# Kernel optimization log

Hardware: AMD Instinct MI355X
Metric: run time of the kernel (lower is better)

Reference implementation:

```python
import jax, jax.numpy as jnp
import numpy as np

NUM_HEADS = 12

def setup_inputs() -> dict:
    key = jax.random.key(0)
    k1, k2, k3 = jax.random.split(key, 3)
    B, N, C = 8, 1024, 768
    x = jax.random.normal(k1, (B, N, C), dtype=jnp.float32)
    Wqkv = jax.random.normal(k2, (C, 3 * C), dtype=jnp.float32) * (C ** -0.5)
    bqkv = jnp.zeros((3 * C,), dtype=jnp.float32)
    Wproj = jax.random.normal(k3, (C, C), dtype=jnp.float32) * (C ** -0.5)
    bproj = jnp.zeros((C,), dtype=jnp.float32)
    return {"x": x, "Wqkv": Wqkv, "bqkv": bqkv, "Wproj": Wproj, "bproj": bproj}

def reference(x, Wqkv, bqkv, Wproj, bproj):
    B, N, C = x.shape
    H = NUM_HEADS
    D = C // H
    scale = D ** -0.5
    qkv = x @ Wqkv + bqkv                       # [B,N,3C]
    qkv = qkv.reshape(B, N, 3, H, D)
    q, k, v = qkv[:, :, 0], qkv[:, :, 1], qkv[:, :, 2]  # [B,N,H,D]
    attn = jnp.einsum('bnhd,bmhd->bhnm', q, k) * scale  # [B,H,N,N]
    attn = jax.nn.softmax(attn, axis=-1)
    # dropout is identity in eval mode
    out = jnp.einsum('bhnm,bmhd->bnhd', attn, v).reshape(B, N, C)
    out = out @ Wproj + bproj
    return out
```

## Files before the change

kernel.cpp:

```cpp
#include <hip/hip_runtime.h>
#include <hip/hip_bf16.h>
#include <cstdint>
#include <cstddef>

typedef __bf16 bf16;
typedef __bf16 bf16x8 __attribute__((ext_vector_type(8)));
typedef __bf16 bf16x4 __attribute__((ext_vector_type(4)));
typedef __bf16 bf16x2 __attribute__((ext_vector_type(2)));
typedef float f32x4 __attribute__((ext_vector_type(4)));
typedef float f32x16 __attribute__((ext_vector_type(16)));
typedef unsigned int u32;
typedef u32 u32x4 __attribute__((ext_vector_type(4)));

#define LDS_CAST(p) (__attribute__((address_space(3))) void*)(p)
#define GLB_CAST(p) (const __attribute__((address_space(1))) void*)(p)
#define MFMA16(a, b, c) __builtin_amdgcn_mfma_f32_16x16x32_bf16(a, b, c, 0, 0, 0)
#define MFMA32(a, b, c) __builtin_amdgcn_mfma_f32_32x32x16_bf16(a, b, c, 0, 0, 0)

#if __has_builtin(__builtin_amdgcn_exp2f)
#define EXPF(x) __builtin_amdgcn_exp2f(x)
#define QK_SCALE 0.18033688011112042f
#else
#define EXPF(x) __expf(x)
#define QK_SCALE 0.125f
#endif

static constexpr int BATCH = 8;
static constexpr int NSEQ  = 1024;
static constexpr int CDIM  = 768;
static constexpr int NH    = 12;
static constexpr int HD    = 64;
static constexpr int MTOT  = BATCH * NSEQ;
static constexpr int NC3   = 3 * CDIM;

static constexpr float M_FIX = 12.0f;

__device__ inline u32 pkbf(float a, float b) {
    bf16x2 t = { (bf16)a, (bf16)b };
    return __builtin_bit_cast(u32, t);
}

__global__ void cast_kernel(const float* __restrict__ src, bf16* __restrict__ dst, int n4) {
    int i = blockIdx.x * blockDim.x + threadIdx.x;
    if (i < n4) {
        float4 v = ((const float4*)src)[i];
        bf16x4 o = { (bf16)v.x, (bf16)v.y, (bf16)v.z, (bf16)v.w };
        ((bf16x4*)dst)[i] = o;
    }
}

__global__ void tcast_kernel(const float* __restrict__ src, bf16* __restrict__ dst,
                             int K, int N) {
    __shared__ float tile[32][33];
    const int n0 = blockIdx.x * 32, k0 = blockIdx.y * 32;
    const int tx = threadIdx.x & 31, ty = threadIdx.x >> 5;
#pragma unroll
    for (int p = 0; p < 4; p++)
        tile[ty + p * 8][tx] = src[(size_t)(k0 + ty + p * 8) * N + n0 + tx];
    __syncthreads();
#pragma unroll
    for (int p = 0; p < 4; p++)
        dst[(size_t)(n0 + ty + p * 8) * K + k0 + tx] = (bf16)tile[tx][ty + p * 8];
}

template <int MODE>
__global__ __launch_bounds__(512, 4) void gemm_kernel(
    const bf16* __restrict__ A, const bf16* __restrict__ Bt,
    const float* __restrict__ bias, float* __restrict__ outf,
    bf16* __restrict__ q, bf16* __restrict__ kk, bf16* __restrict__ v,
    int Ndim, int K)
{
    __shared__ alignas(16) bf16 sAB[3][12288];
    const int tid  = threadIdx.x;
    const int lane = tid & 63;
    const int quad = lane >> 4;
    const int l16  = lane & 15;
    const int wid  = tid >> 6;
    const int wmI  = wid >> 1;
    const int wnI  = wid & 1;

    const int wg = blockIdx.x;
    const int x  = (wg & 7) * (gridDim.x >> 3) + (wg >> 3);
    const int nTn = Ndim >> 7;
    const int tn = x % nTn, tm = x / nTn;
    const int tmB = tm << 8, tnB = tn << 7;

    int aoff[4], boff[4];
    {
        const int xr = ((quad ^ (l16 & 3)) << 3);
#pragma unroll
        for (int i = 0; i < 4; i++) aoff[i] = (wmI * 64 + i * 16 + l16) * 32 + xr;
#pragma unroll
        for (int j = 0; j < 4; j++) boff[j] = 8192 + (wnI * 64 + j * 16 + l16) * 32 + xr;
    }

    const int r0 = tid >> 2;
    const int c0 = (tid & 3) ^ (r0 & 3);
    const bf16* gA0 = A  + (size_t)(tmB + r0) * K + c0 * 8;
    const bf16* gA1 = gA0 + (size_t)128 * K;
    const bf16* gB0 = Bt + (size_t)(tnB + r0) * K + c0 * 8;
    const int ldsb = (tid & 448) * 8;

    auto STAGE = [&](int t, int bsel) {
        const int k0 = t << 5;
        bf16* d = &sAB[bsel][0];
        __builtin_amdgcn_global_load_lds(GLB_CAST(gA0 + k0), LDS_CAST(d + ldsb),        16, 0, 0);
        __builtin_amdgcn_global_load_lds(GLB_CAST(gA1 + k0), LDS_CAST(d + 4096 + ldsb), 16, 0, 0);
        __builtin_amdgcn_global_load_lds(GLB_CAST(gB0 + k0), LDS_CAST(d + 8192 + ldsb), 16, 0, 0);
    };

    const f32x4 fzero = {0.f, 0.f, 0.f, 0.f};
    f32x4 acc[4][4];
#pragma unroll
    for (int i = 0; i < 4; i++)
#pragma unroll
        for (int j = 0; j < 4; j++) acc[i][j] = fzero;

    const int NT = K >> 5;
    STAGE(0, 0);
    STAGE(1, 1);
    asm volatile("s_waitcnt vmcnt(3)" ::: "memory");
    __builtin_amdgcn_sched_barrier(0);
    __builtin_amdgcn_s_barrier();

    int bsel = 0;
    for (int t = 0; t < NT; ++t) {
        int b2 = bsel + 2; if (b2 >= 3) b2 -= 3;
        if (t + 2 < NT) STAGE(t + 2, b2);

        const bf16* buf = &sAB[bsel][0];
        bf16x8 af[4], bfr[4];
#pragma unroll
        for (int i = 0; i < 4; i++) af[i]  = *(const bf16x8*)(buf + aoff[i]);
#pragma unroll
        for (int j = 0; j < 4; j++) bfr[j] = *(const bf16x8*)(buf + boff[j]);

        __builtin_amdgcn_s_setprio(1);
#pragma unroll
        for (int i = 0; i < 4; i++)
#pragma unroll
            for (int j = 0; j < 4; j++) acc[i][j] = MFMA16(af[i], bfr[j], acc[i][j]);
        __builtin_amdgcn_s_setprio(0);

        if (t < NT - 1) {
            if (t + 2 < NT) asm volatile("s_waitcnt vmcnt(3)" ::: "memory");
            else            asm volatile("s_waitcnt vmcnt(0)" ::: "memory");
            __builtin_amdgcn_sched_barrier(0);
            __builtin_amdgcn_s_barrier();
            __builtin_amdgcn_sched_barrier(0);
        }
        bsel += 1; if (bsel >= 3) bsel -= 3;
    }

    if (MODE == 0) {
#pragma unroll
        for (int i = 0; i < 4; i++) {
            int row = tmB + wmI * 64 + i * 16 + quad * 4;
#pragma unroll
            for (int j = 0; j < 4; j++) {
                int col = tnB + wnI * 64 + j * 16 + l16;
                float bv = bias[col];
                float* op = outf + (size_t)row * Ndim + col;
#pragma unroll
                for (int r = 0; r < 4; r++) op[(size_t)r * Ndim] = acc[i][j][r] + bv;
            }
        }
    } else {
#pragma unroll
        for (int i = 0; i < 4; i++) {
            int row = tmB + wmI * 64 + i * 16 + quad * 4;
            int b  = row >> 10;
            int ns = row & 1023;
#pragma unroll
            for (int j = 0; j < 4; j++) {
                int col = tnB + wnI * 64 + j * 16 + l16;
                int t3  = col / 768;
                int rem = col - t3 * 768;
                int h = rem >> 6;
                int d = rem & 63;
                float bv = bias[col];
                if (t3 == 0) {
                    bf16* qp = q + ((size_t)(b * NH + h) * NSEQ + ns) * HD + d;
#pragma unroll
                    for (int r = 0; r < 4; r++)
                        qp[(size_t)r * HD] = (bf16)((acc[i][j][r] + bv) * (float)QK_SCALE);
                } else if (t3 == 1) {
                    bf16* kp = kk + ((size_t)(b * NH + h) * NSEQ + ns) * HD + d;
#pragma unroll
                    for (int r = 0; r < 4; r++) kp[(size_t)r * HD] = (bf16)(acc[i][j][r] + bv);
                } else {
                    bf16x4 pv = { (bf16)(acc[i][j][0] + bv), (bf16)(acc[i][j][1] + bv),
                                  (bf16)(acc[i][j][2] + bv), (bf16)(acc[i][j][3] + bv) };
                    *(bf16x4*)(v + ((size_t)(b * NH + h) * HD + d) * NSEQ + ns) = pv;
                }
            }
        }
    }
}

__global__ __launch_bounds__(256) void attn_kernel(
    const bf16* __restrict__ q, const bf16* __restrict__ k,
    const bf16* __restrict__ v, bf16* __restrict__ o)
{
    __shared__ alignas(16) bf16 sKV[2][8192];
    const int tid  = threadIdx.x;
    const int lane = tid & 63;
    const int w    = tid >> 6;
    const int h    = lane >> 5;
    const int l32  = lane & 31;

    const int wg  = blockIdx.x;
    const int xcd = wg & 7;
    const int idx = wg >> 3;
    const int bh  = xcd * 12 + (idx % 12);
    const int qt  = idx / 12;
    const int b = bh / NH, hh = bh - b * NH;

    const bf16* qb = q + ((size_t)bh * NSEQ + qt * 128) * HD;
    const bf16* kb = k + (size_t)bh * NSEQ * HD;
    const bf16* vb = v + (size_t)bh * HD * NSEQ;

#pragma unroll
    for (int i = 0; i < 4; i++) {
        int slot = w * 256 + i * 64 + lane;
        int r = slot >> 3, cs = slot & 7;
        __builtin_amdgcn_global_load_lds(GLB_CAST(qb + r * HD + ((cs ^ (r & 7)) * 8)),
                                         LDS_CAST(&sKV[1][(w * 256 + i * 64) * 8]), 16, 0, 0);
    }
    auto stageKV = [&](int kt, int buf) {
#pragma unroll
        for (int i = 0; i < 2; i++) {
            int slot = w * 128 + i * 64 + lane;
            int r = slot >> 3, cs = slot & 7;
            int cc = (cs ^ (r & 7)) * 8;
            __builtin_amdgcn_global_load_lds(GLB_CAST(kb + (size_t)(kt * 64 + r) * HD + cc),
                                             LDS_CAST(&sKV[buf][(w * 128 + i * 64) * 8]), 16, 0, 0);
            __builtin_amdgcn_global_load_lds(GLB_CAST(vb + (size_t)r * NSEQ + kt * 64 + cc),
                                             LDS_CAST(&sKV[buf][4096 + (w * 128 + i * 64) * 8]), 16, 0, 0);
        }
    };
    stageKV(0, 0);
    __syncthreads();

    bf16x8 qf[4];
    {
        int row = w * 32 + l32, rx = row & 7;
#pragma unroll
        for (int cd = 0; cd < 4; cd++)
            qf[cd] = *(const bf16x8*)(&sKV[1][(row * 8 + ((2 * cd + h) ^ rx)) * 8]);
    }

    bf16x8 onesA;
#pragma unroll
    for (int i = 0; i < 8; i++) onesA[i] = (bf16)1.0f;

    f32x16 accO[2], accL;
#pragma unroll
    for (int dt = 0; dt < 2; dt++)
#pragma unroll
        for (int i = 0; i < 16; i++) accO[dt][i] = 0.f;
#pragma unroll
    for (int i = 0; i < 16; i++) accL[i] = 0.f;

    for (int kt = 0; kt < 16; kt++) {
        const int cur = kt & 1;
        __syncthreads();
        if (kt < 15) stageKV(kt + 1, 1 - cur);
        const bf16* sKc = &sKV[cur][0];
        const bf16* sVc = &sKV[cur][4096];

        f32x16 accS[2];
#pragma unroll
        for (int kvt = 0; kvt < 2; kvt++)
#pragma unroll
            for (int i = 0; i < 16; i++) accS[kvt][i] = 0.f;
        __builtin_amdgcn_s_setprio(1);
#pragma unroll
        for (int kvt = 0; kvt < 2; kvt++) {
            int row = kvt * 32 + l32, rx = row & 7;
#pragma unroll
            for (int cd = 0; cd < 4; cd++) {
                bf16x8 kf = *(const bf16x8*)(sKc + (row * 8 + ((2 * cd + h) ^ rx)) * 8);
                accS[kvt] = MFMA32(kf, qf[cd], accS[kvt]);
            }
        }
        __builtin_amdgcn_s_setprio(0);

        u32 pr[2][4][2];
#pragma unroll
        for (int kvt = 0; kvt < 2; kvt++)
#pragma unroll
            for (int g = 0; g < 4; g++) {
                pr[kvt][g][0] = pkbf(EXPF(accS[kvt][4 * g + 0] - M_FIX),
                                     EXPF(accS[kvt][4 * g + 1] - M_FIX));
                pr[kvt][g][1] = pkbf(EXPF(accS[kvt][4 * g + 2] - M_FIX),
                                     EXPF(accS[kvt][4 * g + 3] - M_FIX));
            }

        bf16x8 pf[4];
#pragma unroll
        for (int c = 0; c < 4; c++) {
            int kvt = c >> 1, c1 = c & 1;
            u32 u00 = pr[kvt][2 * c1][0],     u01 = pr[kvt][2 * c1][1];
            u32 u10 = pr[kvt][2 * c1 + 1][0], u11 = pr[kvt][2 * c1 + 1][1];
            u32 y0 = h ? u10 : u00, y1 = h ? u11 : u01;
            u32 z0 = h ? u00 : u10, z1 = h ? u01 : u11;
            u32 w0 = (u32)__shfl_xor((int)z0, 32);
            u32 w1 = (u32)__shfl_xor((int)z1, 32);
            u32x4 fv = { h ? w0 : y0, h ? w1 : y1, h ? y0 : w0, h ? y1 : w1 };
            pf[c] = __builtin_bit_cast(bf16x8, fv);
        }

        __builtin_amdgcn_s_setprio(1);
#pragma unroll
        for (int dt = 0; dt < 2; dt++) {
            int row = dt * 32 + l32, rx = row & 7;
#pragma unroll
            for (int c = 0; c < 4; c++) {
                bf16x8 vf = *(const bf16x8*)(sVc + (row * 8 + ((2 * c + h) ^ rx)) * 8);
                accO[dt] = MFMA32(vf, pf[c], accO[dt]);
            }
        }
#pragma unroll
        for (int c = 0; c < 4; c++) accL = MFMA32(onesA, pf[c], accL);
        __builtin_amdgcn_s_setprio(0);
    }

    float inv = 1.f / accL[0];
    bf16* ob = o + ((size_t)b * NSEQ + qt * 128 + w * 32 + l32) * CDIM + hh * HD;
#pragma unroll
    for (int dt = 0; dt < 2; dt++)
#pragma unroll
        for (int g = 0; g < 4; g++) {
            bf16x4 t = { (bf16)(accO[dt][4 * g + 0] * inv), (bf16)(accO[dt][4 * g + 1] * inv),
                         (bf16)(accO[dt][4 * g + 2] * inv), (bf16)(accO[dt][4 * g + 3] * inv) };
            *(bf16x4*)(ob + dt * 32 + 8 * g + 4 * h) = t;
        }
}

extern "C" void kernel_launch(void* const* d_in, const int* in_sizes, int n_in,
                              void* d_out, int out_size, void* d_ws, size_t ws_size,
                              hipStream_t stream)
{
    const float* x     = (const float*)d_in[0];
    const float* Wqkv  = (const float*)d_in[1];
    const float* bqkv  = (const float*)d_in[2];
    const float* Wproj = (const float*)d_in[3];
    const float* bproj = (const float*)d_in[4];
    float* out = (float*)d_out;

    char* ws = (char*)d_ws;
    const size_t MC2 = (size_t)MTOT * CDIM * 2;
    bf16* xb     = (bf16*)ws; ws += MC2;
    bf16* wqkvt  = (bf16*)ws; ws += (size_t)NC3 * CDIM * 2;
    bf16* wprojt = (bf16*)ws; ws += (size_t)CDIM * CDIM * 2;
    bf16* qw     = (bf16*)ws; ws += MC2;
    bf16* kw     = (bf16*)ws; ws += MC2;
    bf16* vw     = (bf16*)ws; ws += MC2;
    bf16* ow     = (bf16*)ws; ws += MC2;

    int n4 = MTOT * CDIM / 4;
    cast_kernel<<<dim3((n4 + 255) / 256), dim3(256), 0, stream>>>(x, xb, n4);
    tcast_kernel<<<dim3(NC3 / 32, CDIM / 32), dim3(256), 0, stream>>>(Wqkv,  wqkvt,  CDIM, NC3);
    tcast_kernel<<<dim3(CDIM / 32, CDIM / 32), dim3(256), 0, stream>>>(Wproj, wprojt, CDIM, CDIM);

    gemm_kernel<1><<<dim3((NC3 / 128) * (MTOT / 256)), dim3(512), 0, stream>>>(
        xb, wqkvt, bqkv, nullptr, qw, kw, vw, NC3, CDIM);

    attn_kernel<<<dim3(768), dim3(256), 0, stream>>>(qw, kw, vw, ow);

    gemm_kernel<0><<<dim3((CDIM / 128) * (MTOT / 256)), dim3(512), 0, stream>>>(
        ow, wprojt, bproj, out, nullptr, nullptr, nullptr, CDIM, CDIM);
}
```

Baseline: 202.5 us.

## Template GEMM on M tile size, use 128-row tiles for projection, double-buffer

Adds a BM template parameter to the GEMM so the output-projection GEMM uses 128x128 tiles with 256 threads, doubling its grid to better fill the CUs. The GEMM pipeline also changes from a 3-stage ring with partial vmcnt waits to a simpler double buffer that waits for all loads at the top of each iteration. This cuts LDS use but exposes more load latency, and the change also applies to the QKV GEMM.

```diff
diff --git a/kernel.cpp b/kernel.cpp
--- a/kernel.cpp
+++ b/kernel.cpp
@@ -63,14 +63,15 @@
         dst[(size_t)(n0 + ty + p * 8) * K + k0 + tx] = (bf16)tile[tx][ty + p * 8];
 }
 
-template <int MODE>
-__global__ __launch_bounds__(512, 4) void gemm_kernel(
+template <int MODE, int BM>
+__global__ __launch_bounds__(BM * 2, 4) void gemm_kernel(
     const bf16* __restrict__ A, const bf16* __restrict__ Bt,
     const float* __restrict__ bias, float* __restrict__ outf,
     bf16* __restrict__ q, bf16* __restrict__ kk, bf16* __restrict__ v,
     int Ndim, int K)
 {
-    __shared__ alignas(16) bf16 sAB[3][12288];
+    constexpr int BN = 128;
+    __shared__ alignas(16) bf16 sAB[2][(BM + BN) * 32];
     const int tid  = threadIdx.x;
     const int lane = tid & 63;
     const int quad = lane >> 4;
@@ -83,7 +84,7 @@
     const int x  = (wg & 7) * (gridDim.x >> 3) + (wg >> 3);
     const int nTn = Ndim >> 7;
     const int tn = x % nTn, tm = x / nTn;
-    const int tmB = tm << 8, tnB = tn << 7;
+    const int tmB = tm * BM, tnB = tn * BN;
 
     int aoff[4], boff[4];
     {
@@ -91,22 +92,30 @@
 #pragma unroll
         for (int i = 0; i < 4; i++) aoff[i] = (wmI * 64 + i * 16 + l16) * 32 + xr;
 #pragma unroll
-        for (int j = 0; j < 4; j++) boff[j] = 8192 + (wnI * 64 + j * 16 + l16) * 32 + xr;
+        for (int j = 0; j < 4; j++) boff[j] = BM * 32 + (wnI * 64 + j * 16 + l16) * 32 + xr;
     }
 
     const int r0 = tid >> 2;
     const int c0 = (tid & 3) ^ (r0 & 3);
     const bf16* gA0 = A  + (size_t)(tmB + r0) * K + c0 * 8;
-    const bf16* gA1 = gA0 + (size_t)128 * K;
+    const bf16* gA1 = gA0 + (size_t)(BM / 2) * K;
     const bf16* gB0 = Bt + (size_t)(tnB + r0) * K + c0 * 8;
-    const int ldsb = (tid & 448) * 8;
+    const bf16* gB1 = gB0 + (size_t)64 * K;
+    const int ldsb = (tid & ~63) * 8;
 
     auto STAGE = [&](int t, int bsel) {
         const int k0 = t << 5;
-        bf16* d = &sAB[bsel][0];
-        __builtin_amdgcn_global_load_lds(GLB_CAST(gA0 + k0), LDS_CAST(d + ldsb),        16, 0, 0);
-        __builtin_amdgcn_global_load_lds(GLB_CAST(gA1 + k0), LDS_CAST(d + 4096 + ldsb), 16, 0, 0);
-        __builtin_amdgcn_global_load_lds(GLB_CAST(gB0 + k0), LDS_CAST(d + 8192 + ldsb), 16, 0, 0);
+        bf16* d = &sAB[bsel][0] + ldsb;
+        if constexpr (BM == 256) {
+            __builtin_amdgcn_global_load_lds(GLB_CAST(gA0 + k0), LDS_CAST(d),        16, 0, 0);
+            __builtin_amdgcn_global_load_lds(GLB_CAST(gA1 + k0), LDS_CAST(d + 4096), 16, 0, 0);
+            __builtin_amdgcn_global_load_lds(GLB_CAST(gB0 + k0), LDS_CAST(d + 8192), 16, 0, 0);
+        } else {
+            __builtin_amdgcn_global_load_lds(GLB_CAST(gA0 + k0), LDS_CAST(d),        16, 0, 0);
+            __builtin_amdgcn_global_load_lds(GLB_CAST(gA1 + k0), LDS_CAST(d + 2048), 16, 0, 0);
+            __builtin_amdgcn_global_load_lds(GLB_CAST(gB0 + k0), LDS_CAST(d + 4096), 16, 0, 0);
+            __builtin_amdgcn_global_load_lds(GLB_CAST(gB1 + k0), LDS_CAST(d + 6144), 16, 0, 0);
+        }
     };
 
     const f32x4 fzero = {0.f, 0.f, 0.f, 0.f};
@@ -118,15 +127,13 @@
 
     const int NT = K >> 5;
     STAGE(0, 0);
-    STAGE(1, 1);
-    asm volatile("s_waitcnt vmcnt(3)" ::: "memory");
-    __builtin_amdgcn_sched_barrier(0);
-    __builtin_amdgcn_s_barrier();
 
     int bsel = 0;
     for (int t = 0; t < NT; ++t) {
-        int b2 = bsel + 2; if (b2 >= 3) b2 -= 3;
-        if (t + 2 < NT) STAGE(t + 2, b2);
+        asm volatile("s_waitcnt vmcnt(0)" ::: "memory");
+        __builtin_amdgcn_sched_barrier(0);
+        __builtin_amdgcn_s_barrier();
+        if (t + 1 < NT) STAGE(t + 1, bsel ^ 1);
 
         const bf16* buf = &sAB[bsel][0];
         bf16x8 af[4], bfr[4];
@@ -141,15 +148,7 @@
 #pragma unroll
             for (int j = 0; j < 4; j++) acc[i][j] = MFMA16(af[i], bfr[j], acc[i][j]);
         __builtin_amdgcn_s_setprio(0);
-
-        if (t < NT - 1) {
-            if (t + 2 < NT) asm volatile("s_waitcnt vmcnt(3)" ::: "memory");
-            else            asm volatile("s_waitcnt vmcnt(0)" ::: "memory");
-            __builtin_amdgcn_sched_barrier(0);
-            __builtin_amdgcn_s_barrier();
-            __builtin_amdgcn_sched_barrier(0);
-        }
-        bsel += 1; if (bsel >= 3) bsel -= 3;
+        bsel ^= 1;
     }
 
     if (MODE == 0) {
@@ -364,11 +363,11 @@
     tcast_kernel<<<dim3(NC3 / 32, CDIM / 32), dim3(256), 0, stream>>>(Wqkv,  wqkvt,  CDIM, NC3);
     tcast_kernel<<<dim3(CDIM / 32, CDIM / 32), dim3(256), 0, stream>>>(Wproj, wprojt, CDIM, CDIM);
 
-    gemm_kernel<1><<<dim3((NC3 / 128) * (MTOT / 256)), dim3(512), 0, stream>>>(
+    gemm_kernel<1, 256><<<dim3((NC3 / 128) * (MTOT / 256)), dim3(512), 0, stream>>>(
         xb, wqkvt, bqkv, nullptr, qw, kw, vw, NC3, CDIM);
 
     attn_kernel<<<dim3(768), dim3(256), 0, stream>>>(qw, kw, vw, ow);
 
-    gemm_kernel<0><<<dim3((CDIM / 128) * (MTOT / 256)), dim3(512), 0, stream>>>(
+    gemm_kernel<0, 128><<<dim3((CDIM / 128) * (MTOT / 128)), dim3(256), 0, stream>>>(
         ow, wprojt, bproj, out, nullptr, nullptr, nullptr, CDIM, CDIM);
 }
```

New measurement: 202.2 us. Within noise of the previous version (-0.1%).
